# Performance work log

Measured on AMD Instinct MI355X. Metric: run time of the kernel, lower is better.

The kernel has to match this reference:

```python
import jax, jax.numpy as jnp
import numpy as np

B, T, E = 4, 2048, 1024
H = 16
DH = E // H
SCALE = DH ** -0.5


def setup_inputs() -> dict:
    key = jax.random.key(0)
    ks = jax.random.split(key, 5)
    # small init scale for weights to keep softmax well-conditioned
    return {
        "x": jax.random.normal(ks[0], (B, T, E), dtype=jnp.float32),
        "w_qkv": jax.random.normal(ks[1], (3 * E, E), dtype=jnp.float32) * 0.02,
        "b_qkv": jax.random.normal(ks[2], (3 * E,), dtype=jnp.float32) * 0.02,
        "w_proj": jax.random.normal(ks[3], (E, E), dtype=jnp.float32) * 0.02,
        "b_proj": jax.random.normal(ks[4], (E,), dtype=jnp.float32) * 0.02,
    }


def reference(x, w_qkv, b_qkv, w_proj, b_proj):
    Bs, Ts, Es = x.shape
    # fused qkv projection (torch Linear: y = x W^T + b)
    qkv = x @ w_qkv.T + b_qkv                       # [B,T,3E]
    qkv = qkv.reshape(Bs, Ts, 3, H, DH)
    q, k, v = qkv[:, :, 0], qkv[:, :, 1], qkv[:, :, 2]  # [B,T,H,DH]
    # scores: materialize full TxT matrix per head, as in the original
    scores = jnp.einsum("bthd,bshd->bhts", q, k) * SCALE  # [B,H,T,T]
    causal = jnp.tril(jnp.ones((Ts, Ts), dtype=bool))
    scores = jnp.where(causal[None, None], scores, jnp.float32(-jnp.inf))
    attn = jax.nn.softmax(scores, axis=-1)
    # dropout = 0.0 (eval / deterministic reference)
    out = jnp.einsum("bhts,bshd->bthd", attn, v)    # [B,T,H,DH]
    out = out.reshape(Bs, Ts, Es)
    return out @ w_proj.T + b_proj
```

## Files before the change

### kernel.cpp

```cpp
#include <hip/hip_runtime.h>
#include <hip/hip_bf16.h>

#define B_ 4
#define T_ 2048
#define E_ 1024
#define H_ 16
#define DH_ 64
#define QSCALE_ 0.18033688f

typedef __attribute__((ext_vector_type(8))) short bf16x8;
typedef __attribute__((ext_vector_type(4))) float f32x4;
typedef unsigned int u32;

__device__ inline ushort f2bf(float f) {
    union { float f; unsigned u; } v; v.f = f;
    unsigned r = (v.u + 0x7fffu + ((v.u >> 16) & 1u)) >> 16;
    return (ushort)r;
}

__device__ inline u32 pack2bf(float a, float b) {
    union { float f; u32 u; } ua, ub; ua.f = a; ub.f = b;
    return __builtin_amdgcn_perm(ub.u, ua.u, 0x07060302);
}

__device__ inline void gload16(const ushort* g, ushort* l) {
    __builtin_amdgcn_global_load_lds((const __attribute__((address_space(1))) u32*)g,
                                     (__attribute__((address_space(3))) u32*)l, 16, 0, 0);
}

__global__ void cvt_all(const float* __restrict__ x, const float* __restrict__ wq,
                        const float* __restrict__ wp,
                        ushort* __restrict__ xo, ushort* __restrict__ wqo, ushort* __restrict__ wpo)
{
    const int NX = B_ * T_ * E_ / 4;
    const int NW = 3 * E_ * E_ / 4;
    int i = blockIdx.x * 256 + threadIdx.x;
    const float* s; ushort* d; int off;
    if (i < NX)            { s = x;  d = xo;  off = i; }
    else if (i < NX + NW)  { s = wq; d = wqo; off = i - NX; }
    else                   { s = wp; d = wpo; off = i - NX - NW; }
    float4 f = ((const float4*)s)[off];
    ushort4 u;
    u.x = f2bf(f.x); u.y = f2bf(f.y); u.z = f2bf(f.z); u.w = f2bf(f.w);
    ((ushort4*)d)[off] = u;
}

__global__ __launch_bounds__(256) void gemm_qkv(
    const ushort* __restrict__ Xb, const ushort* __restrict__ Wb,
    const float* __restrict__ bias,
    ushort* __restrict__ Q, ushort* __restrict__ K, ushort* __restrict__ Vt)
{
    __shared__ ushort As[128 * 32];
    __shared__ ushort Bs[128 * 32];
    const int m0 = blockIdx.x * 128;
    const int n0 = blockIdx.y * 128;
    const int kind = n0 >> 10;
    const int tid  = threadIdx.x;
    const int wave = tid >> 6, lane = tid & 63;
    const int lrow = lane & 15, quad = lane >> 4;
    const int srow = lane >> 2, scol = (lane & 3) * 8;

    const ushort* gA0 = Xb + (size_t)(m0 + wave * 32 + srow) * 1024 + scol;
    const ushort* gA1 = gA0 + (size_t)16 * 1024;
    const ushort* gB0 = Wb + (size_t)(n0 + wave * 32 + srow) * 1024 + scol;
    const ushort* gB1 = gB0 + (size_t)16 * 1024;
    ushort* lA0 = &As[(wave * 32) * 32];
    ushort* lA1 = &As[(wave * 32 + 16) * 32];
    ushort* lB0 = &Bs[(wave * 32) * 32];
    ushort* lB1 = &Bs[(wave * 32 + 16) * 32];

    const int mw = (wave >> 1) * 64, nw = (wave & 1) * 64;

    f32x4 acc[4][4];
#pragma unroll
    for (int i = 0; i < 4; i++)
#pragma unroll
        for (int j = 0; j < 4; j++) acc[i][j] = f32x4{0.f, 0.f, 0.f, 0.f};

    const int b = m0 >> 11;

    if (kind != 2) {
        for (int k0 = 0; k0 < 1024; k0 += 32) {
            __syncthreads();
            gload16(gA0 + k0, lA0);
            gload16(gA1 + k0, lA1);
            gload16(gB0 + k0, lB0);
            gload16(gB1 + k0, lB1);
            __syncthreads();
            bf16x8 a[4], bfr[4];
#pragma unroll
            for (int i = 0; i < 4; i++)
                a[i] = *(const bf16x8*)&As[(mw + i * 16 + lrow) * 32 + quad * 8];
#pragma unroll
            for (int j = 0; j < 4; j++)
                bfr[j] = *(const bf16x8*)&Bs[(nw + j * 16 + lrow) * 32 + quad * 8];
#pragma unroll
            for (int i = 0; i < 4; i++)
#pragma unroll
                for (int j = 0; j < 4; j++)
                    acc[i][j] = __builtin_amdgcn_mfma_f32_16x16x32_bf16(bfr[j], a[i], acc[i][j], 0, 0, 0);
        }
        ushort* dst = (kind == 0) ? Q : K;
        const float scale = (kind == 0) ? QSCALE_ : 1.f;
#pragma unroll
        for (int j = 0; j < 4; j++) {
            int nq = (n0 & 1023) + nw + j * 16 + quad * 4;
            int h = nq >> 6, d = nq & 63;
            float4 bv = *(const float4*)&bias[n0 + nw + j * 16 + quad * 4];
            size_t bh = (size_t)(b * H_ + h);
#pragma unroll
            for (int i = 0; i < 4; i++) {
                int t = (m0 + mw + i * 16 + lrow) & 2047;
                ushort4 o;
                o.x = f2bf((acc[i][j][0] + bv.x) * scale);
                o.y = f2bf((acc[i][j][1] + bv.y) * scale);
                o.z = f2bf((acc[i][j][2] + bv.z) * scale);
                o.w = f2bf((acc[i][j][3] + bv.w) * scale);
                *(ushort4*)&dst[(bh * T_ + t) * DH_ + d] = o;
            }
        }
    } else {
        for (int k0 = 0; k0 < 1024; k0 += 32) {
            __syncthreads();
            gload16(gA0 + k0, lA0);
            gload16(gA1 + k0, lA1);
            gload16(gB0 + k0, lB0);
            gload16(gB1 + k0, lB1);
            __syncthreads();
            bf16x8 a[4], bfr[4];
#pragma unroll
            for (int i = 0; i < 4; i++)
                a[i] = *(const bf16x8*)&As[(mw + i * 16 + lrow) * 32 + quad * 8];
#pragma unroll
            for (int j = 0; j < 4; j++)
                bfr[j] = *(const bf16x8*)&Bs[(nw + j * 16 + lrow) * 32 + quad * 8];
#pragma unroll
            for (int i = 0; i < 4; i++)
#pragma unroll
                for (int j = 0; j < 4; j++)
                    acc[i][j] = __builtin_amdgcn_mfma_f32_16x16x32_bf16(a[i], bfr[j], acc[i][j], 0, 0, 0);
        }
#pragma unroll
        for (int j = 0; j < 4; j++) {
            int nv = (n0 & 1023) + nw + j * 16 + lrow;
            int h = nv >> 6, d = nv & 63;
            float bv = bias[n0 + nw + j * 16 + lrow];
            size_t bh = (size_t)(b * H_ + h);
#pragma unroll
            for (int i = 0; i < 4; i++) {
                int t = (m0 + mw + i * 16 + quad * 4) & 2047;
                ushort4 o;
                o.x = f2bf(acc[i][j][0] + bv);
                o.y = f2bf(acc[i][j][1] + bv);
                o.z = f2bf(acc[i][j][2] + bv);
                o.w = f2bf(acc[i][j][3] + bv);
                *(ushort4*)&Vt[(bh * DH_ + d) * T_ + t] = o;
            }
        }
    }
}

#define LDT_ 76

__global__ __launch_bounds__(256) void flash_attn(
    const ushort* __restrict__ Q, const ushort* __restrict__ K,
    const ushort* __restrict__ Vg,
    ushort* __restrict__ O)
{
    __shared__ ushort Ks[64 * LDT_];
    __shared__ ushort Vt[64 * LDT_];
    __shared__ ushort Ps[128 * LDT_];

    const int qtA = 15 - blockIdx.x;
    const int qtB = blockIdx.x;
    const int bh = blockIdx.y;
    const int tid  = threadIdx.x;
    const int wave = tid >> 6, lane = tid & 63;
    const int lrow = lane & 15, quad = lane >> 4;
    const int sr = tid >> 2, sc = (tid & 3) * 16;

    const ushort* Qbh = Q  + (size_t)bh * T_ * DH_;
    const ushort* Kbh = K  + (size_t)bh * T_ * DH_;
    const ushort* Vbh = Vg + (size_t)bh * DH_ * T_;
    const int b_ = bh >> 4, h_ = bh & 15;

    auto stageQ = [&](int qt, bf16x8 qa[2][2]) {
        int qr = tid >> 1, qc = (tid & 1) * 32;
        const ushort* src = &Qbh[(size_t)(qt * 128 + qr) * DH_ + qc];
#pragma unroll
        for (int i = 0; i < 4; i++)
            *(int4*)&Ps[qr * LDT_ + qc + 8 * i] = *(const int4*)&src[8 * i];
        __syncthreads();
#pragma unroll
        for (int s = 0; s < 2; s++)
#pragma unroll
            for (int h = 0; h < 2; h++)
                qa[s][h] = *(const bf16x8*)&Ps[(s * 64 + wave * 16 + lrow) * LDT_ + h * 32 + quad * 8];
    };

    bf16x8 qaA[2][2], qaB[2][2];
    stageQ(qtA, qaA);
    __syncthreads();
    stageQ(qtB, qaB);

    auto run = [&](const bf16x8 (&qa)[2][2], int qt) {
        const int lastkt = 2 * qt + 1;

        int4 kr0 = *(const int4*)&Kbh[(size_t)sr * DH_ + sc];
        int4 kr1 = *(const int4*)&Kbh[(size_t)sr * DH_ + sc + 8];
        int4 vr0 = *(const int4*)&Vbh[(size_t)sr * T_ + sc];
        int4 vr1 = *(const int4*)&Vbh[(size_t)sr * T_ + sc + 8];

        float ls[2] = {0.f, 0.f};
        f32x4 accO[2][4];
#pragma unroll
        for (int s = 0; s < 2; s++)
#pragma unroll
            for (int j = 0; j < 4; j++) accO[s][j] = f32x4{0.f, 0.f, 0.f, 0.f};

        for (int kt = 0; kt <= lastkt; ++kt) {
            __syncthreads();
            *(int4*)&Ks[sr * LDT_ + sc]     = kr0;
            *(int4*)&Ks[sr * LDT_ + sc + 8] = kr1;
            *(int4*)&Vt[sr * LDT_ + sc]     = vr0;
            *(int4*)&Vt[sr * LDT_ + sc + 8] = vr1;
            __syncthreads();
            if (kt < lastkt) {
                kr0 = *(const int4*)&Kbh[(size_t)((kt + 1) * 64 + sr) * DH_ + sc];
                kr1 = *(const int4*)&Kbh[(size_t)((kt + 1) * 64 + sr) * DH_ + sc + 8];
                vr0 = *(const int4*)&Vbh[(size_t)sr * T_ + (kt + 1) * 64 + sc];
                vr1 = *(const int4*)&Vbh[(size_t)sr * T_ + (kt + 1) * 64 + sc + 8];
            }

            bf16x8 kb0[4], kb1[4];
#pragma unroll
            for (int j = 0; j < 4; j++) {
                kb0[j] = *(const bf16x8*)&Ks[(j * 16 + lrow) * LDT_ + quad * 8];
                kb1[j] = *(const bf16x8*)&Ks[(j * 16 + lrow) * LDT_ + 32 + quad * 8];
            }

            const bool do0 = (kt != lastkt);
#pragma unroll
            for (int s = 0; s < 2; s++) {
                if (s == 0 && !do0) continue;
                f32x4 st[4];
#pragma unroll
                for (int j = 0; j < 4; j++) {
                    f32x4 sj = f32x4{0.f, 0.f, 0.f, 0.f};
                    sj = __builtin_amdgcn_mfma_f32_16x16x32_bf16(kb0[j], qa[s][0], sj, 0, 0, 0);
                    sj = __builtin_amdgcn_mfma_f32_16x16x32_bf16(kb1[j], qa[s][1], sj, 0, 0, 0);
                    st[j] = sj;
                }
                if (kt == 2 * qt + s) {
                    const int qrow = qt * 128 + s * 64 + wave * 16 + lrow;
                    const int keyb = kt * 64 + quad * 4;
#pragma unroll
                    for (int j = 0; j < 4; j++)
#pragma unroll
                        for (int r = 0; r < 4; r++)
                            if (keyb + j * 16 + r > qrow) st[j][r] = -1e30f;
                }
                float lp = 0.f;
#pragma unroll
                for (int j = 0; j < 4; j++)
#pragma unroll
                    for (int r = 0; r < 4; r++) {
                        float p = __builtin_amdgcn_exp2f(st[j][r]);
                        st[j][r] = p;
                        lp += p;
                    }
                ls[s] += lp;
                ushort* prow = &Ps[(s * 64 + wave * 16 + lrow) * LDT_ + quad * 4];
#pragma unroll
                for (int j = 0; j < 4; j++) {
                    *(u32*)&prow[j * 16]     = pack2bf(st[j][0], st[j][1]);
                    *(u32*)&prow[j * 16 + 2] = pack2bf(st[j][2], st[j][3]);
                }
            }

            bf16x8 vb0[4], vb1[4];
#pragma unroll
            for (int j = 0; j < 4; j++) {
                vb0[j] = *(const bf16x8*)&Vt[(j * 16 + lrow) * LDT_ + quad * 8];
                vb1[j] = *(const bf16x8*)&Vt[(j * 16 + lrow) * LDT_ + 32 + quad * 8];
            }
#pragma unroll
            for (int s = 0; s < 2; s++) {
                if (s == 0 && !do0) continue;
                bf16x8 pa0 = *(const bf16x8*)&Ps[(s * 64 + wave * 16 + lrow) * LDT_ + quad * 8];
                bf16x8 pa1 = *(const bf16x8*)&Ps[(s * 64 + wave * 16 + lrow) * LDT_ + 32 + quad * 8];
#pragma unroll
                for (int jd = 0; jd < 4; jd++) {
                    accO[s][jd] = __builtin_amdgcn_mfma_f32_16x16x32_bf16(pa0, vb0[jd], accO[s][jd], 0, 0, 0);
                    accO[s][jd] = __builtin_amdgcn_mfma_f32_16x16x32_bf16(pa1, vb1[jd], accO[s][jd], 0, 0, 0);
                }
            }
        }

#pragma unroll
        for (int s = 0; s < 2; s++) {
            ls[s] += __shfl_xor(ls[s], 16, 64);
            ls[s] += __shfl_xor(ls[s], 32, 64);
        }
#pragma unroll
        for (int s = 0; s < 2; s++) {
#pragma unroll
            for (int r = 0; r < 4; r++) {
                float lv = __shfl(ls[s], quad * 4 + r, 64);
                float inv = 1.f / lv;
                int t = qt * 128 + s * 64 + wave * 16 + quad * 4 + r;
#pragma unroll
                for (int jd = 0; jd < 4; jd++) {
                    int d = jd * 16 + lrow;
                    O[((size_t)(b_ * T_ + t)) * E_ + h_ * DH_ + d] = f2bf(accO[s][jd][r] * inv);
                }
            }
        }
    };

    run(qaA, qtA);
    run(qaB, qtB);
}

__global__ __launch_bounds__(256) void gemm_proj(
    const ushort* __restrict__ Ob, const ushort* __restrict__ Wb,
    const float* __restrict__ bias, float* __restrict__ out)
{
    __shared__ ushort As[128 * 32];
    __shared__ ushort Bs[128 * 32];
    const int m0 = blockIdx.x * 128;
    const int n0 = blockIdx.y * 128;
    const int tid  = threadIdx.x;
    const int wave = tid >> 6, lane = tid & 63;
    const int lrow = lane & 15, quad = lane >> 4;
    const int srow = lane >> 2, scol = (lane & 3) * 8;

    const ushort* gA0 = Ob + (size_t)(m0 + wave * 32 + srow) * 1024 + scol;
    const ushort* gA1 = gA0 + (size_t)16 * 1024;
    const ushort* gB0 = Wb + (size_t)(n0 + wave * 32 + srow) * 1024 + scol;
    const ushort* gB1 = gB0 + (size_t)16 * 1024;
    ushort* lA0 = &As[(wave * 32) * 32];
    ushort* lA1 = &As[(wave * 32 + 16) * 32];
    ushort* lB0 = &Bs[(wave * 32) * 32];
    ushort* lB1 = &Bs[(wave * 32 + 16) * 32];

    const int mw = (wave >> 1) * 64, nw = (wave & 1) * 64;

    f32x4 acc[4][4];
#pragma unroll
    for (int i = 0; i < 4; i++)
#pragma unroll
        for (int j = 0; j < 4; j++) acc[i][j] = f32x4{0.f, 0.f, 0.f, 0.f};

    for (int k0 = 0; k0 < 1024; k0 += 32) {
        __syncthreads();
        gload16(gA0 + k0, lA0);
        gload16(gA1 + k0, lA1);
        gload16(gB0 + k0, lB0);
        gload16(gB1 + k0, lB1);
        __syncthreads();
        bf16x8 a[4], bfr[4];
#pragma unroll
        for (int i = 0; i < 4; i++)
            a[i] = *(const bf16x8*)&As[(mw + i * 16 + lrow) * 32 + quad * 8];
#pragma unroll
        for (int j = 0; j < 4; j++)
            bfr[j] = *(const bf16x8*)&Bs[(nw + j * 16 + lrow) * 32 + quad * 8];
#pragma unroll
        for (int i = 0; i < 4; i++)
#pragma unroll
            for (int j = 0; j < 4; j++)
                acc[i][j] = __builtin_amdgcn_mfma_f32_16x16x32_bf16(bfr[j], a[i], acc[i][j], 0, 0, 0);
    }

#pragma unroll
    for (int j = 0; j < 4; j++) {
        int n = n0 + nw + j * 16 + quad * 4;
        float4 bv = *(const float4*)&bias[n];
#pragma unroll
        for (int i = 0; i < 4; i++) {
            int m = m0 + mw + i * 16 + lrow;
            float4 o;
            o.x = acc[i][j][0] + bv.x;
            o.y = acc[i][j][1] + bv.y;
            o.z = acc[i][j][2] + bv.z;
            o.w = acc[i][j][3] + bv.w;
            *(float4*)&out[(size_t)m * 1024 + n] = o;
        }
    }
}

extern "C" void kernel_launch(void* const* d_in, const int* in_sizes, int n_in,
                              void* d_out, int out_size, void* d_ws, size_t ws_size,
                              hipStream_t stream) {
    const float* x      = (const float*)d_in[0];
    const float* w_qkv  = (const float*)d_in[1];
    const float* b_qkv  = (const float*)d_in[2];
    const float* w_proj = (const float*)d_in[3];
    const float* b_proj = (const float*)d_in[4];
    float* out = (float*)d_out;

    char* ws = (char*)d_ws;
    ushort* Xb     = (ushort*)ws; ws += (size_t)B_ * T_ * E_ * 2;
    ushort* Wqkvb  = (ushort*)ws; ws += (size_t)3 * E_ * E_ * 2;
    ushort* Wprojb = (ushort*)ws; ws += (size_t)E_ * E_ * 2;
    ushort* Qb     = (ushort*)ws; ws += (size_t)B_ * H_ * T_ * DH_ * 2;
    ushort* Kb     = (ushort*)ws; ws += (size_t)B_ * H_ * T_ * DH_ * 2;
    ushort* Vtb    = (ushort*)ws; ws += (size_t)B_ * H_ * T_ * DH_ * 2;
    ushort* Ob     = (ushort*)ws; ws += (size_t)B_ * T_ * E_ * 2;

    int ntot = (B_ * T_ * E_ + 3 * E_ * E_ + E_ * E_) / 4;
    cvt_all<<<ntot / 256, 256, 0, stream>>>(x, w_qkv, w_proj, Xb, Wqkvb, Wprojb);

    gemm_qkv<<<dim3(64, 24), 256, 0, stream>>>(Xb, Wqkvb, b_qkv, Qb, Kb, Vtb);
    flash_attn<<<dim3(8, 64), 256, 0, stream>>>(Qb, Kb, Vtb, Ob);
    gemm_proj<<<dim3(64, 8), 256, 0, stream>>>(Ob, Wprojb, b_proj, out);
}
```

Before: 258.9 us.

## Keep P in registers via transposed PV MFMA, widen K/V tiles to 128

The attention kernel no longer writes the softmax probabilities P to shared memory. It computes O^T = V^T P^T with 16x16x16 bf16 MFMAs, so the score accumulator layout feeds straight into the B operand. K/V staging now loads 128 keys per round instead of 64, which halves the barrier pairs per key range, and the output is stored as ushort4 vectors. The costs are more, smaller MFMA instructions (or a zero-padded emulation if the 1k builtin is missing), a larger V LDS footprint, and more registers for the prefetch buffers.

```diff
diff --git a/kernel.cpp b/kernel.cpp
--- a/kernel.cpp
+++ b/kernel.cpp
@@ -9,6 +9,7 @@
 #define QSCALE_ 0.18033688f
 
 typedef __attribute__((ext_vector_type(8))) short bf16x8;
+typedef __attribute__((ext_vector_type(4))) short bf16x4;
 typedef __attribute__((ext_vector_type(4))) float f32x4;
 typedef unsigned int u32;
 
@@ -22,6 +23,17 @@
     union { float f; u32 u; } ua, ub; ua.f = a; ub.f = b;
     return __builtin_amdgcn_perm(ub.u, ua.u, 0x07060302);
 }
+
+#if __has_builtin(__builtin_amdgcn_mfma_f32_16x16x16bf16_1k)
+#define MFMA16(A, B, C) __builtin_amdgcn_mfma_f32_16x16x16bf16_1k(A, B, C, 0, 0, 0)
+#else
+__device__ inline f32x4 mfma16_emul(bf16x4 a, bf16x4 b, f32x4 c) {
+    bf16x8 a8 = {a[0], a[1], a[2], a[3], 0, 0, 0, 0};
+    bf16x8 b8 = {b[0], b[1], b[2], b[3], 0, 0, 0, 0};
+    return __builtin_amdgcn_mfma_f32_16x16x32_bf16(a8, b8, c, 0, 0, 0);
+}
+#define MFMA16(A, B, C) mfma16_emul(A, B, C)
+#endif
 
 __device__ inline void gload16(const ushort* g, ushort* l) {
     __builtin_amdgcn_global_load_lds((const __attribute__((address_space(1))) u32*)g,
@@ -160,16 +172,16 @@
     }
 }
 
-#define LDT_ 76
+#define LDK_ 76
+#define LDV_ 136
 
 __global__ __launch_bounds__(256) void flash_attn(
     const ushort* __restrict__ Q, const ushort* __restrict__ K,
     const ushort* __restrict__ Vg,
     ushort* __restrict__ O)
 {
-    __shared__ ushort Ks[64 * LDT_];
-    __shared__ ushort Vt[64 * LDT_];
-    __shared__ ushort Ps[128 * LDT_];
+    __shared__ ushort Ks[128 * LDK_];
+    __shared__ ushort Vt[64 * LDV_];
 
     const int qtA = 15 - blockIdx.x;
     const int qtB = blockIdx.x;
@@ -177,25 +189,26 @@
     const int tid  = threadIdx.x;
     const int wave = tid >> 6, lane = tid & 63;
     const int lrow = lane & 15, quad = lane >> 4;
-    const int sr = tid >> 2, sc = (tid & 3) * 16;
 
     const ushort* Qbh = Q  + (size_t)bh * T_ * DH_;
     const ushort* Kbh = K  + (size_t)bh * T_ * DH_;
     const ushort* Vbh = Vg + (size_t)bh * DH_ * T_;
     const int b_ = bh >> 4, h_ = bh & 15;
 
+    const int kq = tid >> 1, kc = (tid & 1) * 32;
+    const int vd = tid >> 2, vc = (tid & 3) * 32;
+
     auto stageQ = [&](int qt, bf16x8 qa[2][2]) {
-        int qr = tid >> 1, qc = (tid & 1) * 32;
-        const ushort* src = &Qbh[(size_t)(qt * 128 + qr) * DH_ + qc];
+        const ushort* src = &Qbh[(size_t)(qt * 128 + kq) * DH_ + kc];
 #pragma unroll
         for (int i = 0; i < 4; i++)
-            *(int4*)&Ps[qr * LDT_ + qc + 8 * i] = *(const int4*)&src[8 * i];
+            *(int4*)&Ks[kq * LDK_ + kc + 8 * i] = *(const int4*)&src[8 * i];
         __syncthreads();
 #pragma unroll
         for (int s = 0; s < 2; s++)
 #pragma unroll
             for (int h = 0; h < 2; h++)
-                qa[s][h] = *(const bf16x8*)&Ps[(s * 64 + wave * 16 + lrow) * LDT_ + h * 32 + quad * 8];
+                qa[s][h] = *(const bf16x8*)&Ks[(s * 64 + wave * 16 + lrow) * LDK_ + h * 32 + quad * 8];
     };
 
     bf16x8 qaA[2][2], qaB[2][2];
@@ -204,95 +217,100 @@
     stageQ(qtB, qaB);
 
     auto run = [&](const bf16x8 (&qa)[2][2], int qt) {
-        const int lastkt = 2 * qt + 1;
-
-        int4 kr0 = *(const int4*)&Kbh[(size_t)sr * DH_ + sc];
-        int4 kr1 = *(const int4*)&Kbh[(size_t)sr * DH_ + sc + 8];
-        int4 vr0 = *(const int4*)&Vbh[(size_t)sr * T_ + sc];
-        int4 vr1 = *(const int4*)&Vbh[(size_t)sr * T_ + sc + 8];
+        const int rounds = qt + 1;
+        const int lastTile = 2 * qt + 1;
+
+        int4 kr[4], vr[4];
+#pragma unroll
+        for (int i = 0; i < 4; i++) {
+            kr[i] = *(const int4*)&Kbh[(size_t)kq * DH_ + kc + 8 * i];
+            vr[i] = *(const int4*)&Vbh[(size_t)vd * T_ + vc + 8 * i];
+        }
 
         float ls[2] = {0.f, 0.f};
-        f32x4 accO[2][4];
+        f32x4 accOT[2][4];
 #pragma unroll
         for (int s = 0; s < 2; s++)
 #pragma unroll
-            for (int j = 0; j < 4; j++) accO[s][j] = f32x4{0.f, 0.f, 0.f, 0.f};
-
-        for (int kt = 0; kt <= lastkt; ++kt) {
-            __syncthreads();
-            *(int4*)&Ks[sr * LDT_ + sc]     = kr0;
-            *(int4*)&Ks[sr * LDT_ + sc + 8] = kr1;
-            *(int4*)&Vt[sr * LDT_ + sc]     = vr0;
-            *(int4*)&Vt[sr * LDT_ + sc + 8] = vr1;
-            __syncthreads();
-            if (kt < lastkt) {
-                kr0 = *(const int4*)&Kbh[(size_t)((kt + 1) * 64 + sr) * DH_ + sc];
-                kr1 = *(const int4*)&Kbh[(size_t)((kt + 1) * 64 + sr) * DH_ + sc + 8];
-                vr0 = *(const int4*)&Vbh[(size_t)sr * T_ + (kt + 1) * 64 + sc];
-                vr1 = *(const int4*)&Vbh[(size_t)sr * T_ + (kt + 1) * 64 + sc + 8];
-            }
-
-            bf16x8 kb0[4], kb1[4];
-#pragma unroll
-            for (int j = 0; j < 4; j++) {
-                kb0[j] = *(const bf16x8*)&Ks[(j * 16 + lrow) * LDT_ + quad * 8];
-                kb1[j] = *(const bf16x8*)&Ks[(j * 16 + lrow) * LDT_ + 32 + quad * 8];
-            }
-
-            const bool do0 = (kt != lastkt);
-#pragma unroll
-            for (int s = 0; s < 2; s++) {
-                if (s == 0 && !do0) continue;
-                f32x4 st[4];
+            for (int j = 0; j < 4; j++) accOT[s][j] = f32x4{0.f, 0.f, 0.f, 0.f};
+
+        for (int r2 = 0; r2 < rounds; ++r2) {
+            __syncthreads();
+#pragma unroll
+            for (int i = 0; i < 4; i++) {
+                *(int4*)&Ks[kq * LDK_ + kc + 8 * i] = kr[i];
+                *(int4*)&Vt[vd * LDV_ + vc + 8 * i] = vr[i];
+            }
+            __syncthreads();
+            if (r2 + 1 < rounds) {
+#pragma unroll
+                for (int i = 0; i < 4; i++) {
+                    kr[i] = *(const int4*)&Kbh[(size_t)((r2 + 1) * 128 + kq) * DH_ + kc + 8 * i];
+                    vr[i] = *(const int4*)&Vbh[(size_t)vd * T_ + (r2 + 1) * 128 + vc + 8 * i];
+                }
+            }
+
+#pragma unroll
+            for (int h = 0; h < 2; ++h) {
+                const int tile = 2 * r2 + h;
+                const bool act0 = (tile != lastTile);
+
+                bf16x8 kb0[4], kb1[4];
 #pragma unroll
                 for (int j = 0; j < 4; j++) {
-                    f32x4 sj = f32x4{0.f, 0.f, 0.f, 0.f};
-                    sj = __builtin_amdgcn_mfma_f32_16x16x32_bf16(kb0[j], qa[s][0], sj, 0, 0, 0);
-                    sj = __builtin_amdgcn_mfma_f32_16x16x32_bf16(kb1[j], qa[s][1], sj, 0, 0, 0);
-                    st[j] = sj;
+                    kb0[j] = *(const bf16x8*)&Ks[(h * 64 + j * 16 + lrow) * LDK_ + quad * 8];
+                    kb1[j] = *(const bf16x8*)&Ks[(h * 64 + j * 16 + lrow) * LDK_ + 32 + quad * 8];
                 }
-                if (kt == 2 * qt + s) {
-                    const int qrow = qt * 128 + s * 64 + wave * 16 + lrow;
-                    const int keyb = kt * 64 + quad * 4;
+
+                f32x4 st[2][4];
+#pragma unroll
+                for (int s = 0; s < 2; s++) {
+                    if (s == 0 && !act0) continue;
+#pragma unroll
+                    for (int j = 0; j < 4; j++) {
+                        f32x4 sj = f32x4{0.f, 0.f, 0.f, 0.f};
+                        sj = __builtin_amdgcn_mfma_f32_16x16x32_bf16(kb0[j], qa[s][0], sj, 0, 0, 0);
+                        sj = __builtin_amdgcn_mfma_f32_16x16x32_bf16(kb1[j], qa[s][1], sj, 0, 0, 0);
+                        st[s][j] = sj;
+                    }
+                    if (tile == 2 * qt + s) {
+                        const int qrow = qt * 128 + s * 64 + wave * 16 + lrow;
+                        const int keyb = tile * 64 + quad * 4;
+#pragma unroll
+                        for (int j = 0; j < 4; j++)
+#pragma unroll
+                            for (int r = 0; r < 4; r++)
+                                if (keyb + j * 16 + r > qrow) st[s][j][r] = -1e30f;
+                    }
+                    float lp = 0.f;
 #pragma unroll
                     for (int j = 0; j < 4; j++)
 #pragma unroll
-                        for (int r = 0; r < 4; r++)
-                            if (keyb + j * 16 + r > qrow) st[j][r] = -1e30f;
+                        for (int r = 0; r < 4; r++) {
+                            float p = __builtin_amdgcn_exp2f(st[s][j][r]);
+                            st[s][j][r] = p;
+                            lp += p;
+                        }
+                    ls[s] += lp;
                 }
-                float lp = 0.f;
-#pragma unroll
-                for (int j = 0; j < 4; j++)
-#pragma unroll
-                    for (int r = 0; r < 4; r++) {
-                        float p = __builtin_amdgcn_exp2f(st[j][r]);
-                        st[j][r] = p;
-                        lp += p;
+
+#pragma unroll
+                for (int kg = 0; kg < 4; ++kg) {
+                    bf16x4 va[4];
+#pragma unroll
+                    for (int jd = 0; jd < 4; jd++)
+                        va[jd] = *(const bf16x4*)&Vt[(jd * 16 + lrow) * LDV_ + h * 64 + kg * 16 + quad * 4];
+#pragma unroll
+                    for (int s = 0; s < 2; s++) {
+                        if (s == 0 && !act0) continue;
+                        union { u32 u[2]; bf16x4 v; } pu;
+                        pu.u[0] = pack2bf(st[s][kg][0], st[s][kg][1]);
+                        pu.u[1] = pack2bf(st[s][kg][2], st[s][kg][3]);
+                        bf16x4 pb = pu.v;
+#pragma unroll
+                        for (int jd = 0; jd < 4; jd++)
+                            accOT[s][jd] = MFMA16(va[jd], pb, accOT[s][jd]);
                     }
-                ls[s] += lp;
-                ushort* prow = &Ps[(s * 64 + wave * 16 + lrow) * LDT_ + quad * 4];
-#pragma unroll
-                for (int j = 0; j < 4; j++) {
-                    *(u32*)&prow[j * 16]     = pack2bf(st[j][0], st[j][1]);
-                    *(u32*)&prow[j * 16 + 2] = pack2bf(st[j][2], st[j][3]);
-                }
-            }
-
-            bf16x8 vb0[4], vb1[4];
-#pragma unroll
-            for (int j = 0; j < 4; j++) {
-                vb0[j] = *(const bf16x8*)&Vt[(j * 16 + lrow) * LDT_ + quad * 8];
-                vb1[j] = *(const bf16x8*)&Vt[(j * 16 + lrow) * LDT_ + 32 + quad * 8];
-            }
-#pragma unroll
-            for (int s = 0; s < 2; s++) {
-                if (s == 0 && !do0) continue;
-                bf16x8 pa0 = *(const bf16x8*)&Ps[(s * 64 + wave * 16 + lrow) * LDT_ + quad * 8];
-                bf16x8 pa1 = *(const bf16x8*)&Ps[(s * 64 + wave * 16 + lrow) * LDT_ + 32 + quad * 8];
-#pragma unroll
-                for (int jd = 0; jd < 4; jd++) {
-                    accO[s][jd] = __builtin_amdgcn_mfma_f32_16x16x32_bf16(pa0, vb0[jd], accO[s][jd], 0, 0, 0);
-                    accO[s][jd] = __builtin_amdgcn_mfma_f32_16x16x32_bf16(pa1, vb1[jd], accO[s][jd], 0, 0, 0);
                 }
             }
         }
@@ -304,16 +322,17 @@
         }
 #pragma unroll
         for (int s = 0; s < 2; s++) {
-#pragma unroll
-            for (int r = 0; r < 4; r++) {
-                float lv = __shfl(ls[s], quad * 4 + r, 64);
-                float inv = 1.f / lv;
-                int t = qt * 128 + s * 64 + wave * 16 + quad * 4 + r;
-#pragma unroll
-                for (int jd = 0; jd < 4; jd++) {
-                    int d = jd * 16 + lrow;
-                    O[((size_t)(b_ * T_ + t)) * E_ + h_ * DH_ + d] = f2bf(accO[s][jd][r] * inv);
-                }
+            float inv = 1.f / ls[s];
+            int t = qt * 128 + s * 64 + wave * 16 + lrow;
+            ushort* orow = &O[((size_t)(b_ * T_ + t)) * E_ + h_ * DH_ + quad * 4];
+#pragma unroll
+            for (int jd = 0; jd < 4; jd++) {
+                ushort4 o;
+                o.x = f2bf(accOT[s][jd][0] * inv);
+                o.y = f2bf(accOT[s][jd][1] * inv);
+                o.z = f2bf(accOT[s][jd][2] * inv);
+                o.w = f2bf(accOT[s][jd][3] * inv);
+                *(ushort4*)&orow[jd * 16] = o;
             }
         }
     };
```

After: 316.1 us. +22.1%, slower.
